# Optimization experiments

Measured on AMD Instinct MI355X. Metric: run time of the kernel, lower is better.

The kernel has to match this reference:

```python
import jax, jax.numpy as jnp
import numpy as np

B, C, D, H, K = 512, 112, 128, 8, 8  # batch, channels(=seq), d_model, heads, conv kernel
HD = D // H
SCALE = HD ** -0.5
BN_EPS = 1e-5
LN_EPS = 1e-5


def setup_inputs() -> dict:
    key = jax.random.key(0)
    ks = jax.random.split(key, 12)
    s = 0.05
    return {
        "x": jax.random.normal(ks[0], (B, C, D), jnp.float32),
        "conv_w": jax.random.normal(ks[1], (C, 1, K), jnp.float32) * s,
        "conv_b": jax.random.normal(ks[2], (C,), jnp.float32) * s,
        "bn_g": jnp.ones((C,), jnp.float32),
        "bn_b": jnp.zeros((C,), jnp.float32),
        "bn_m": jnp.zeros((C,), jnp.float32),
        "bn_v": jnp.ones((C,), jnp.float32),
        "wq": jax.random.normal(ks[3], (D, D), jnp.float32) * s,
        "bq": jax.random.normal(ks[4], (D,), jnp.float32) * s,
        "wk": jax.random.normal(ks[5], (D, D), jnp.float32) * s,
        "bk": jax.random.normal(ks[6], (D,), jnp.float32) * s,
        "wv": jax.random.normal(ks[7], (D, D), jnp.float32) * s,
        "bv": jax.random.normal(ks[8], (D,), jnp.float32) * s,
        "wo": jax.random.normal(ks[9], (D, D), jnp.float32) * s,
        "bo": jax.random.normal(ks[10], (D,), jnp.float32) * s,
        "ln_g": jnp.ones((D,), jnp.float32),
        "ln_b": jnp.zeros((D,), jnp.float32),
    }


def _forward(x, conv_w, conv_b, bn_g, bn_b, bn_m, bn_v,
             wq, bq, wk, bk, wv, bv, wo, bo, ln_g, ln_b):
    # resnet_1: depthwise Conv1d(padding='same', k=8) -> GELU -> BatchNorm1d (eval)
    # torch 'same' padding for even k: left = (k-1)//2 = 3, right = 4
    h = jax.lax.conv_general_dilated(
        x, conv_w, window_strides=(1,), padding=[(3, 4)],
        dimension_numbers=("NCH", "OIH", "NCH"), feature_group_count=C)
    h = h + conv_b[None, :, None]
    h = jax.nn.gelu(h, approximate=False)
    h = (h - bn_m[None, :, None]) * (bn_g[None, :, None] * jax.lax.rsqrt(bn_v + BN_EPS)[None, :, None]) + bn_b[None, :, None]
    src = x + h  # [B, C, D]; attention treats C as sequence dim

    # multi-head attention (hand-rolled, res_attention path with prev=None)
    q = (src @ wq.T + bq).reshape(B, C, H, HD).transpose(0, 2, 1, 3)  # [B,H,S,hd]
    k = (src @ wk.T + bk).reshape(B, C, H, HD).transpose(0, 2, 1, 3)
    v = (src @ wv.T + bv).reshape(B, C, H, HD).transpose(0, 2, 1, 3)
    scores = jnp.einsum("bhqd,bhkd->bhqk", q, k) * SCALE  # [B,H,S,S]
    attn = jax.nn.softmax(scores, axis=-1)
    out = jnp.einsum("bhqk,bhkd->bhqd", attn, v)  # [B,H,S,hd]
    out = out.transpose(0, 2, 1, 3).reshape(B, C, D)
    out = out @ wo.T + bo

    # residual + LayerNorm over last dim
    src = src + out
    mu = jnp.mean(src, axis=-1, keepdims=True)
    var = jnp.mean(jnp.square(src - mu), axis=-1, keepdims=True)
    src = (src - mu) * jax.lax.rsqrt(var + LN_EPS) * ln_g + ln_b
    return src


def reference(x, conv_w, conv_b, bn_g, bn_b, bn_m, bn_v,
              wq, bq, wk, bk, wv, bv, wo, bo, ln_g, ln_b):
    return _forward(x, conv_w, conv_b, bn_g, bn_b, bn_m, bn_v,
                    wq, bq, wk, bk, wv, bv, wo, bo, ln_g, ln_b)
```

## Files before the change

kernel.cpp:

```cpp
#include <hip/hip_runtime.h>
#include <hip/hip_bf16.h>

#define BB 512
#define CC 112
#define DD 128
#define HH 8
#define HD 16
#define KK 8

typedef unsigned short u16;
typedef short short8 __attribute__((ext_vector_type(8)));
typedef float f32x4 __attribute__((ext_vector_type(4)));
typedef float f32x16 __attribute__((ext_vector_type(16)));

#define MFMA16(a, b, c) __builtin_amdgcn_mfma_f32_16x16x32_bf16(a, b, c, 0, 0, 0)
#define MFMA32(a, b, c) __builtin_amdgcn_mfma_f32_32x32x16_bf16(a, b, c, 0, 0, 0)

#define PAD 136

__device__ inline u16 f2bf(float f) {
  union { float f; unsigned u; } v{f};
  unsigned r = (v.u + 0x7FFFu + ((v.u >> 16) & 1u)) >> 16;
  return (u16)r;
}
__device__ inline float bf2f(u16 u) {
  union { unsigned u; float f; } v;
  v.u = ((unsigned)u) << 16;
  return v.f;
}
__device__ inline unsigned pk2(float a, float b) {
  __hip_bfloat162 h = __float22bfloat162_rn(float2{a, b});
  union { __hip_bfloat162 h; unsigned u; } v{h};
  return v.u;
}

__global__ __launch_bounds__(256) void k_cqkv(
    const float* __restrict__ x, const float* __restrict__ cw,
    const float* __restrict__ cb, const float* __restrict__ bg,
    const float* __restrict__ bb_, const float* __restrict__ bm,
    const float* __restrict__ bv,
    const float* __restrict__ wq, const float* __restrict__ bq,
    const float* __restrict__ wk, const float* __restrict__ bk,
    const float* __restrict__ wv, const float* __restrict__ bvv,
    u16* __restrict__ src_b, u16* __restrict__ qb, u16* __restrict__ kb,
    u16* __restrict__ vtb) {
  __shared__ u16 sw[128 * PAD];
  const int t = threadIdx.x;
  const int wave = t >> 6, lane = t & 63;
  const int quad = lane >> 4, n = lane & 15;
  const int row_g = blockIdx.x * 64 + wave * 16 + n;
  const int ch = row_g % CC;

  const float4 w0 = *(const float4*)(cw + ch * KK);
  const float4 w1 = *(const float4*)(cw + ch * KK + 4);
  const float cbv = cb[ch];
  const float bscale = bg[ch] * rsqrtf(bv[ch] + 1e-5f);
  const float bmv = bm[ch], bbv = bb_[ch];

  const float* __restrict__ xr = x + (size_t)row_g * DD;
  u16* __restrict__ sbr = src_b + (size_t)row_g * DD;

  short8 A[4];
#pragma unroll
  for (int kf = 0; kf < 4; ++kf) {
    const int c0 = kf * 32 + quad * 8;
    float in[16];
#pragma unroll
    for (int f = 0; f < 4; ++f) {
      const int fi = (c0 >> 2) - 1 + f;
      float4 vv = {0.f, 0.f, 0.f, 0.f};
      if (fi >= 0 && fi < 32) vv = ((const float4*)xr)[fi];
      in[f * 4 + 0] = vv.x; in[f * 4 + 1] = vv.y;
      in[f * 4 + 2] = vv.z; in[f * 4 + 3] = vv.w;
    }
    u16 ob[8];
#pragma unroll
    for (int i = 0; i < 8; ++i) {
      float a = 0.f;
      a = fmaf(in[i + 1], w0.x, a);
      a = fmaf(in[i + 2], w0.y, a);
      a = fmaf(in[i + 3], w0.z, a);
      a = fmaf(in[i + 4], w0.w, a);
      a = fmaf(in[i + 5], w1.x, a);
      a = fmaf(in[i + 6], w1.y, a);
      a = fmaf(in[i + 7], w1.z, a);
      a = fmaf(in[i + 8], w1.w, a);
      a += cbv;
      const float g = 0.5f * a * (1.f + erff(a * 0.70710678118654752440f));
      const float s = in[i + 4] + (g - bmv) * bscale + bbv;
      ob[i] = f2bf(s);
    }
    A[kf] = *(short8*)ob;
    *(short8*)(sbr + c0) = A[kf];
  }

  const int row0w = blockIdx.x * 64 + wave * 16;
  int qk_base[4], vt_base[4];
#pragma unroll
  for (int r = 0; r < 4; ++r) {
    const int g = row0w + quad * 4 + r;
    const int b_ = g / CC, c_ = g - b_ * CC;
    qk_base[r] = (b_ * (HH * CC) + c_) * HD + n;
    vt_base[r] = b_ * (HH * HD * CC) + n * CC + c_;
  }

  const float* const wmats[3] = {wq, wk, wv};
  const float* const biases[3] = {bq, bk, bvv};
  for (int m = 0; m < 3; ++m) {
    __syncthreads();
    {
      const float4* wsrc = (const float4*)wmats[m];
      for (int i = t; i < 4096; i += 256) {
        const int r = i >> 5, c4 = (i & 31) * 4;
        const float4 vv = wsrc[i];
        *(uint2*)&sw[r * PAD + c4] = uint2{pk2(vv.x, vv.y), pk2(vv.z, vv.w)};
      }
    }
    __syncthreads();
    const float* __restrict__ bias = biases[m];
#pragma unroll
    for (int nt = 0; nt < 8; ++nt) {
      f32x4 acc = {0.f, 0.f, 0.f, 0.f};
#pragma unroll
      for (int kf = 0; kf < 4; ++kf) {
        const short8 Bf =
            *(const short8*)&sw[(nt * 16 + n) * PAD + kf * 32 + quad * 8];
        acc = MFMA16(A[kf], Bf, acc);
      }
      const float bcol = bias[nt * 16 + n];
      if (m < 2) {
        u16* __restrict__ o = (m == 0) ? qb : kb;
        const int hoff = nt * (CC * HD);
#pragma unroll
        for (int r = 0; r < 4; ++r)
          o[qk_base[r] + hoff] = f2bf(acc[r] + bcol);
      } else {
        const int hoff = nt * (HD * CC);
#pragma unroll
        for (int r = 0; r < 4; ++r)
          vtb[vt_base[r] + hoff] = f2bf(acc[r] + bcol);
      }
    }
  }
}

__global__ __launch_bounds__(256) void k_attn(
    const u16* __restrict__ qb_, const u16* __restrict__ kb_,
    const u16* __restrict__ vtb_, u16* __restrict__ ab_) {
  const int bh = blockIdx.x;
  const int b = bh >> 3, h = bh & 7;
  const int t = threadIdx.x;
  const int wave = t >> 6;
  const int lane = t & 63;
  const int lo = lane & 31;
  const int hi8 = (lane >> 5) * 8;
  __shared__ u16 VT[HD * PAD];
  __shared__ u16 PL[4 * 32 * PAD];
  const u16* __restrict__ qh = qb_ + (size_t)bh * (CC * HD);
  const u16* __restrict__ kh = kb_ + (size_t)bh * (CC * HD);
  const u16* __restrict__ vth = vtb_ + (size_t)bh * (HD * CC);
  u16* __restrict__ aout = ab_ + (size_t)b * (CC * DD) + h * HD;

  for (int i = t; i < 224; i += 256) {
    const int e = i / 14, c0 = (i - e * 14) * 8;
    *(short8*)&VT[e * PAD + c0] = *(const short8*)(vth + e * CC + c0);
  }
  __syncthreads();

  u16* __restrict__ PW = PL + wave * (32 * PAD);
  const int qt0 = wave * 32;

  short8 Bq = {};
  if (qt0 + lo < CC)
    Bq = *(const short8*)(qh + (qt0 + lo) * HD + hi8);
  f32x16 sa[4];
#pragma unroll
  for (int mt = 0; mt < 4; ++mt) {
    short8 Ak = {};
    const int key = mt * 32 + lo;
    if (key < CC) Ak = *(const short8*)(kh + key * HD + hi8);
    f32x16 z = {};
    sa[mt] = MFMA32(Ak, Bq, z);
  }
  const float C1 = 0.25f * 1.44269504088896341f;
  float mx = -1e30f;
#pragma unroll
  for (int mt = 0; mt < 4; ++mt) {
    const int rmax = (mt == 3) ? 8 : 16;
#pragma unroll
    for (int r = 0; r < 16; ++r)
      if (r < rmax) mx = fmaxf(mx, sa[mt][r]);
  }
  mx = fmaxf(mx, __shfl_xor(mx, 32));
  const float mxc = mx * C1;
  float sum = 0.f;
#pragma unroll
  for (int mt = 0; mt < 4; ++mt) {
    const int rmax = (mt == 3) ? 8 : 16;
#pragma unroll
    for (int r = 0; r < 16; ++r)
      if (r < rmax) {
        const float p = exp2f(fmaf(sa[mt][r], C1, -mxc));
        sa[mt][r] = p;
        sum += p;
      }
  }
  sum += __shfl_xor(sum, 32);
  const float rinv = 1.f / sum;
#pragma unroll
  for (int mt = 0; mt < 4; ++mt) {
    const int nruns = (mt == 3) ? 2 : 4;
#pragma unroll
    for (int run = 0; run < 4; ++run)
      if (run < nruns) {
        const int k0 = mt * 32 + run * 8 + (lane >> 5) * 4;
        const unsigned u0 =
            pk2(sa[mt][4 * run + 0] * rinv, sa[mt][4 * run + 1] * rinv);
        const unsigned u1 =
            pk2(sa[mt][4 * run + 2] * rinv, sa[mt][4 * run + 3] * rinv);
        *(uint2*)&PW[lo * PAD + k0] = uint2{u0, u1};
      }
  }
  __threadfence_block();
  f32x16 oacc = {};
#pragma unroll
  for (int kt = 0; kt < 7; ++kt) {
    const short8 Ap = *(const short8*)&PW[lo * PAD + kt * 16 + hi8];
    short8 Bv = {};
    if (lo < HD) Bv = *(const short8*)&VT[lo * PAD + kt * 16 + hi8];
    oacc = MFMA32(Ap, Bv, oacc);
  }
  if (lo < HD) {
#pragma unroll
    for (int r = 0; r < 16; ++r) {
      const int qrow = qt0 + (r & 3) + 8 * (r >> 2) + 4 * (lane >> 5);
      if (qrow < CC) aout[(size_t)qrow * DD + lo] = f2bf(oacc[r]);
    }
  }
}

__global__ __launch_bounds__(256) void k_out(
    const u16* __restrict__ a_b, const float* __restrict__ wo,
    const float* __restrict__ bo, const u16* __restrict__ src_b,
    const float* __restrict__ lg, const float* __restrict__ lb,
    float* __restrict__ out) {
  __shared__ u16 sw[128 * PAD];
  const int t = threadIdx.x;
  const int wave = t >> 6, lane = t & 63;
  const int quad = lane >> 4, n = lane & 15;
  const int row0 = blockIdx.x * 64 + wave * 16;
  {
    const float4* wsrc = (const float4*)wo;
    for (int i = t; i < 4096; i += 256) {
      const int r = i >> 5, c4 = (i & 31) * 4;
      const float4 vv = wsrc[i];
      *(uint2*)&sw[r * PAD + c4] = uint2{pk2(vv.x, vv.y), pk2(vv.z, vv.w)};
    }
  }
  short8 A[4];
  {
    const size_t rbase = (size_t)(row0 + n) * DD;
#pragma unroll
    for (int kf = 0; kf < 4; ++kf)
      A[kf] = *(const short8*)(a_b + rbase + kf * 32 + quad * 8);
  }
  __syncthreads();
  float v[8][4];
#pragma unroll
  for (int nt = 0; nt < 8; ++nt) {
    f32x4 acc = {0.f, 0.f, 0.f, 0.f};
#pragma unroll
    for (int kf = 0; kf < 4; ++kf) {
      const short8 Bf =
          *(const short8*)&sw[(nt * 16 + n) * PAD + kf * 32 + quad * 8];
      acc = MFMA16(A[kf], Bf, acc);
    }
    const int col = nt * 16 + n;
    const float bcol = bo[col];
#pragma unroll
    for (int r = 0; r < 4; ++r)
      v[nt][r] = acc[r] + bcol +
                 bf2f(src_b[(size_t)(row0 + quad * 4 + r) * DD + col]);
  }
  float sum[4] = {0.f, 0.f, 0.f, 0.f}, sq[4] = {0.f, 0.f, 0.f, 0.f};
#pragma unroll
  for (int nt = 0; nt < 8; ++nt)
#pragma unroll
    for (int r = 0; r < 4; ++r) {
      sum[r] += v[nt][r];
      sq[r] = fmaf(v[nt][r], v[nt][r], sq[r]);
    }
#pragma unroll
  for (int d = 1; d < 16; d <<= 1)
#pragma unroll
    for (int r = 0; r < 4; ++r) {
      sum[r] += __shfl_xor(sum[r], d);
      sq[r] += __shfl_xor(sq[r], d);
    }
  float mu[4], rs[4];
#pragma unroll
  for (int r = 0; r < 4; ++r) {
    mu[r] = sum[r] * (1.f / DD);
    const float var = sq[r] * (1.f / DD) - mu[r] * mu[r];
    rs[r] = rsqrtf(var + 1e-5f);
  }
#pragma unroll
  for (int nt = 0; nt < 8; ++nt) {
    const int col = nt * 16 + n;
    const float g = lg[col], be = lb[col];
#pragma unroll
    for (int r = 0; r < 4; ++r)
      out[(size_t)(row0 + quad * 4 + r) * DD + col] =
          (v[nt][r] - mu[r]) * rs[r] * g + be;
  }
}

extern "C" void kernel_launch(void* const* d_in, const int* in_sizes, int n_in,
                              void* d_out, int out_size, void* d_ws,
                              size_t ws_size, hipStream_t stream) {
  (void)in_sizes; (void)n_in; (void)out_size; (void)ws_size;
  const float* x   = (const float*)d_in[0];
  const float* cw  = (const float*)d_in[1];
  const float* cb  = (const float*)d_in[2];
  const float* bg  = (const float*)d_in[3];
  const float* bb  = (const float*)d_in[4];
  const float* bm  = (const float*)d_in[5];
  const float* bv  = (const float*)d_in[6];
  const float* wq  = (const float*)d_in[7];
  const float* bq  = (const float*)d_in[8];
  const float* wk  = (const float*)d_in[9];
  const float* bk  = (const float*)d_in[10];
  const float* wv  = (const float*)d_in[11];
  const float* bvv = (const float*)d_in[12];
  const float* wo  = (const float*)d_in[13];
  const float* bo  = (const float*)d_in[14];
  const float* lg  = (const float*)d_in[15];
  const float* lb  = (const float*)d_in[16];
  float* out = (float*)d_out;

  const size_t NE = (size_t)BB * CC * DD;
  u16* ub = (u16*)d_ws;
  u16* src_b = ub;
  u16* q_b   = ub + NE;
  u16* k_b   = ub + 2 * NE;
  u16* vt_b  = ub + 3 * NE;
  u16* a_b   = ub + 4 * NE;

  k_cqkv<<<(BB * CC) / 64, 256, 0, stream>>>(
      x, cw, cb, bg, bb, bm, bv, wq, bq, wk, bk, wv, bvv,
      src_b, q_b, k_b, vt_b);
  k_attn<<<BB * HH, 256, 0, stream>>>(q_b, k_b, vt_b, a_b);
  k_out<<<(BB * CC) / 64, 256, 0, stream>>>(a_b, wo, bo, src_b, lg, lb, out);
}
```

Before: 186.2 us.

## Pre-convert weights to bf16 once and drop LDS staging in all kernels

Adds a small kernel that converts wq/wk/wv/wo to bf16 into workspace once per call. The projection and output kernels then read weight fragments straight from global memory (L2-resident) and no longer do per-block fp32 conversion into LDS or the barriers around it. The attention kernel drops its LDS buffers for V and P: the probability fragments are rearranged between lane halves with cross-lane shuffles and V is read directly from global. This trades LDS traffic and barriers for an extra launch, more global/L2 loads and shuffle instructions, but it raises occupancy because the kernels no longer need shared memory.

```diff
diff --git a/kernel.cpp b/kernel.cpp
--- a/kernel.cpp
+++ b/kernel.cpp
@@ -16,8 +16,6 @@
 #define MFMA16(a, b, c) __builtin_amdgcn_mfma_f32_16x16x32_bf16(a, b, c, 0, 0, 0)
 #define MFMA32(a, b, c) __builtin_amdgcn_mfma_f32_32x32x16_bf16(a, b, c, 0, 0, 0)
 
-#define PAD 136
-
 __device__ inline u16 f2bf(float f) {
   union { float f; unsigned u; } v{f};
   unsigned r = (v.u + 0x7FFFu + ((v.u >> 16) & 1u)) >> 16;
@@ -34,17 +32,26 @@
   return v.u;
 }
 
+__global__ __launch_bounds__(256) void k_wcvt(
+    const float* __restrict__ wq, const float* __restrict__ wk,
+    const float* __restrict__ wv, const float* __restrict__ wo,
+    u16* __restrict__ w_b) {
+  const int i = (blockIdx.x * 256 + threadIdx.x);
+  const int sel = i >> 12, off = i & 4095;
+  const float* w = (sel == 0) ? wq : (sel == 1) ? wk : (sel == 2) ? wv : wo;
+  const float4 v = ((const float4*)w)[off];
+  ((uint2*)w_b)[i] = uint2{pk2(v.x, v.y), pk2(v.z, v.w)};
+}
+
 __global__ __launch_bounds__(256) void k_cqkv(
     const float* __restrict__ x, const float* __restrict__ cw,
     const float* __restrict__ cb, const float* __restrict__ bg,
     const float* __restrict__ bb_, const float* __restrict__ bm,
-    const float* __restrict__ bv,
-    const float* __restrict__ wq, const float* __restrict__ bq,
-    const float* __restrict__ wk, const float* __restrict__ bk,
-    const float* __restrict__ wv, const float* __restrict__ bvv,
+    const float* __restrict__ bv, const u16* __restrict__ w_b,
+    const float* __restrict__ bq, const float* __restrict__ bk,
+    const float* __restrict__ bvv,
     u16* __restrict__ src_b, u16* __restrict__ qb, u16* __restrict__ kb,
     u16* __restrict__ vtb) {
-  __shared__ u16 sw[128 * PAD];
   const int t = threadIdx.x;
   const int wave = t >> 6, lane = t & 63;
   const int quad = lane >> 4, n = lane & 15;
@@ -104,19 +111,9 @@
     vt_base[r] = b_ * (HH * HD * CC) + n * CC + c_;
   }
 
-  const float* const wmats[3] = {wq, wk, wv};
   const float* const biases[3] = {bq, bk, bvv};
   for (int m = 0; m < 3; ++m) {
-    __syncthreads();
-    {
-      const float4* wsrc = (const float4*)wmats[m];
-      for (int i = t; i < 4096; i += 256) {
-        const int r = i >> 5, c4 = (i & 31) * 4;
-        const float4 vv = wsrc[i];
-        *(uint2*)&sw[r * PAD + c4] = uint2{pk2(vv.x, vv.y), pk2(vv.z, vv.w)};
-      }
-    }
-    __syncthreads();
+    const u16* __restrict__ wm = w_b + m * 16384;
     const float* __restrict__ bias = biases[m];
 #pragma unroll
     for (int nt = 0; nt < 8; ++nt) {
@@ -124,7 +121,7 @@
 #pragma unroll
       for (int kf = 0; kf < 4; ++kf) {
         const short8 Bf =
-            *(const short8*)&sw[(nt * 16 + n) * PAD + kf * 32 + quad * 8];
+            *(const short8*)(wm + (nt * 16 + n) * DD + kf * 32 + quad * 8);
         acc = MFMA16(A[kf], Bf, acc);
       }
       const float bcol = bias[nt * 16 + n];
@@ -153,26 +150,16 @@
   const int wave = t >> 6;
   const int lane = t & 63;
   const int lo = lane & 31;
-  const int hi8 = (lane >> 5) * 8;
-  __shared__ u16 VT[HD * PAD];
-  __shared__ u16 PL[4 * 32 * PAD];
+  const int hi = lane >> 5;
+  const int hi8 = hi * 8;
   const u16* __restrict__ qh = qb_ + (size_t)bh * (CC * HD);
   const u16* __restrict__ kh = kb_ + (size_t)bh * (CC * HD);
   const u16* __restrict__ vth = vtb_ + (size_t)bh * (HD * CC);
   u16* __restrict__ aout = ab_ + (size_t)b * (CC * DD) + h * HD;
 
-  for (int i = t; i < 224; i += 256) {
-    const int e = i / 14, c0 = (i - e * 14) * 8;
-    *(short8*)&VT[e * PAD + c0] = *(const short8*)(vth + e * CC + c0);
-  }
-  __syncthreads();
-
-  u16* __restrict__ PW = PL + wave * (32 * PAD);
   const int qt0 = wave * 32;
-
   short8 Bq = {};
-  if (qt0 + lo < CC)
-    Bq = *(const short8*)(qh + (qt0 + lo) * HD + hi8);
+  if (qt0 + lo < CC) Bq = *(const short8*)(qh + (qt0 + lo) * HD + hi8);
   f32x16 sa[4];
 #pragma unroll
   for (int mt = 0; mt < 4; ++mt) {
@@ -207,56 +194,55 @@
   }
   sum += __shfl_xor(sum, 32);
   const float rinv = 1.f / sum;
+  unsigned U0[4][4], U1[4][4];
 #pragma unroll
   for (int mt = 0; mt < 4; ++mt) {
-    const int nruns = (mt == 3) ? 2 : 4;
-#pragma unroll
-    for (int run = 0; run < 4; ++run)
-      if (run < nruns) {
-        const int k0 = mt * 32 + run * 8 + (lane >> 5) * 4;
-        const unsigned u0 =
-            pk2(sa[mt][4 * run + 0] * rinv, sa[mt][4 * run + 1] * rinv);
-        const unsigned u1 =
-            pk2(sa[mt][4 * run + 2] * rinv, sa[mt][4 * run + 3] * rinv);
-        *(uint2*)&PW[lo * PAD + k0] = uint2{u0, u1};
+    const int rqmax = (mt == 3) ? 2 : 4;
+#pragma unroll
+    for (int rq = 0; rq < 4; ++rq)
+      if (rq < rqmax) {
+        U0[mt][rq] = pk2(sa[mt][4 * rq + 0] * rinv, sa[mt][4 * rq + 1] * rinv);
+        U1[mt][rq] = pk2(sa[mt][4 * rq + 2] * rinv, sa[mt][4 * rq + 3] * rinv);
       }
   }
-  __threadfence_block();
   f32x16 oacc = {};
 #pragma unroll
   for (int kt = 0; kt < 7; ++kt) {
-    const short8 Ap = *(const short8*)&PW[lo * PAD + kt * 16 + hi8];
+    const int mt = kt >> 1;
+    const int c = 2 * (kt & 1);
+    const unsigned own0 = hi ? U0[mt][c + 1] : U0[mt][c];
+    const unsigned own1 = hi ? U1[mt][c + 1] : U1[mt][c];
+    const unsigned snd0 = hi ? U0[mt][c] : U0[mt][c + 1];
+    const unsigned snd1 = hi ? U1[mt][c] : U1[mt][c + 1];
+    const unsigned got0 = __shfl_xor(snd0, 32);
+    const unsigned got1 = __shfl_xor(snd1, 32);
+    union { unsigned u[4]; short8 s; } ap;
+    ap.u[0] = hi ? got0 : own0;
+    ap.u[1] = hi ? got1 : own1;
+    ap.u[2] = hi ? own0 : got0;
+    ap.u[3] = hi ? own1 : got1;
     short8 Bv = {};
-    if (lo < HD) Bv = *(const short8*)&VT[lo * PAD + kt * 16 + hi8];
-    oacc = MFMA32(Ap, Bv, oacc);
+    if (lo < HD) Bv = *(const short8*)(vth + lo * CC + kt * 16 + hi8);
+    oacc = MFMA32(ap.s, Bv, oacc);
   }
   if (lo < HD) {
 #pragma unroll
     for (int r = 0; r < 16; ++r) {
-      const int qrow = qt0 + (r & 3) + 8 * (r >> 2) + 4 * (lane >> 5);
+      const int qrow = qt0 + (r & 3) + 8 * (r >> 2) + 4 * hi;
       if (qrow < CC) aout[(size_t)qrow * DD + lo] = f2bf(oacc[r]);
     }
   }
 }
 
 __global__ __launch_bounds__(256) void k_out(
-    const u16* __restrict__ a_b, const float* __restrict__ wo,
+    const u16* __restrict__ a_b, const u16* __restrict__ w_bo,
     const float* __restrict__ bo, const u16* __restrict__ src_b,
     const float* __restrict__ lg, const float* __restrict__ lb,
     float* __restrict__ out) {
-  __shared__ u16 sw[128 * PAD];
   const int t = threadIdx.x;
   const int wave = t >> 6, lane = t & 63;
   const int quad = lane >> 4, n = lane & 15;
   const int row0 = blockIdx.x * 64 + wave * 16;
-  {
-    const float4* wsrc = (const float4*)wo;
-    for (int i = t; i < 4096; i += 256) {
-      const int r = i >> 5, c4 = (i & 31) * 4;
-      const float4 vv = wsrc[i];
-      *(uint2*)&sw[r * PAD + c4] = uint2{pk2(vv.x, vv.y), pk2(vv.z, vv.w)};
-    }
-  }
   short8 A[4];
   {
     const size_t rbase = (size_t)(row0 + n) * DD;
@@ -264,7 +250,6 @@
     for (int kf = 0; kf < 4; ++kf)
       A[kf] = *(const short8*)(a_b + rbase + kf * 32 + quad * 8);
   }
-  __syncthreads();
   float v[8][4];
 #pragma unroll
   for (int nt = 0; nt < 8; ++nt) {
@@ -272,7 +257,7 @@
 #pragma unroll
     for (int kf = 0; kf < 4; ++kf) {
       const short8 Bf =
-          *(const short8*)&sw[(nt * 16 + n) * PAD + kf * 32 + quad * 8];
+          *(const short8*)(w_bo + (nt * 16 + n) * DD + kf * 32 + quad * 8);
       acc = MFMA16(A[kf], Bf, acc);
     }
     const int col = nt * 16 + n;
@@ -345,10 +330,12 @@
   u16* k_b   = ub + 2 * NE;
   u16* vt_b  = ub + 3 * NE;
   u16* a_b   = ub + 4 * NE;
-
+  u16* w_b   = ub + 5 * NE;
+
+  k_wcvt<<<64, 256, 0, stream>>>(wq, wk, wv, wo, w_b);
   k_cqkv<<<(BB * CC) / 64, 256, 0, stream>>>(
-      x, cw, cb, bg, bb, bm, bv, wq, bq, wk, bk, wv, bvv,
-      src_b, q_b, k_b, vt_b);
+      x, cw, cb, bg, bb, bm, bv, w_b, bq, bk, bvv, src_b, q_b, k_b, vt_b);
   k_attn<<<BB * HH, 256, 0, stream>>>(q_b, k_b, vt_b, a_b);
-  k_out<<<(BB * CC) / 64, 256, 0, stream>>>(a_b, wo, bo, src_b, lg, lb, out);
-}
+  k_out<<<(BB * CC) / 64, 256, 0, stream>>>(a_b, w_b + 3 * 16384, bo, src_b,
+                                            lg, lb, out);
+}
```

Measured after the change: 214.4 us. 15.1% more time.
